# Optimization experiments

Hardware: AMD Instinct MI355X
Metric: run time of the kernel (lower is better)

Reference implementation:

```python
import jax, jax.numpy as jnp
import numpy as np

L1, L2 = 16, 16            # lattice shape -> translation group
N_SYMM = L1 * L2           # 256 group elements
IN_FEATURES = 32
FEATURES = 64
BATCH = 16


def translation_table(l1, l2):
    """Product table pt[g, h] = index of g^{-1} h for the 2D translation group."""
    n = l1 * l2
    g = np.arange(n)
    a, b = g // l2, g % l2          # coords of g
    c, d = a, b                     # coords of h (same enumeration)
    pt = ((c[None, :] - a[:, None]) % l1) * l2 + ((d[None, :] - b[:, None]) % l2)
    return jnp.asarray(pt, dtype=jnp.int32)  # (n_symm, n_symm)


def setup_inputs() -> dict:
    key = jax.random.key(0)
    kx, kk, kb = jax.random.split(key, 3)
    x = jax.random.normal(kx, (BATCH, IN_FEATURES, N_SYMM), dtype=jnp.float32)
    # default_equivariant_initializer ~ lecun normal, fan_in = in_features * kernel_size
    scale = 1.0 / np.sqrt(IN_FEATURES * N_SYMM)
    kernel = scale * jax.random.normal(kk, (FEATURES, IN_FEATURES, N_SYMM), dtype=jnp.float32)
    bias = jnp.zeros((FEATURES,), dtype=jnp.float32)
    product_table = translation_table(L1, L2)
    return {"x": x, "kernel": kernel, "bias": bias, "product_table": product_table}


def reference(x, kernel, bias, product_table):
    # Expand kernel via group product table: K[f, i, g, h] = kernel[f, i, pt[g, h]]
    # (feature_group_count = 1, mask = None so unmask is identity, kernel_size = n_symm)
    K = jnp.take(kernel, product_table, axis=2)          # (F, I, S, S) -- 536 MB fp32
    # dot_general contracts x dims (in_features, n_symm) with K dims (I, first S)
    out = jnp.einsum('big,figh->bfh', x, K)              # (B, F, S)
    out = out + bias[:, None]                            # bias broadcast over group dim
    return out
```

## Files before the change

### kernel.cpp

```cpp
#include <hip/hip_runtime.h>

typedef unsigned short u16;
typedef unsigned int u32;
typedef __attribute__((ext_vector_type(8))) short bfx8;
typedef __attribute__((ext_vector_type(4))) float fx4;
typedef __attribute__((ext_vector_type(4))) u32 ux4;
typedef __attribute__((ext_vector_type(2))) u32 ux2;

__device__ inline u32 f2bf(float v) {
  u32 u = __builtin_bit_cast(u32, v);
  u = (u + 0x7fffu + ((u >> 16) & 1u)) >> 16;
  return u;
}

__global__ __launch_bounds__(512, 4) void eq_main(const float* __restrict__ xin,
                                                  const float* __restrict__ kin,
                                                  float* __restrict__ part) {
  __shared__ __align__(16) char smem[74752];
  u16* As = (u16*)smem;
  u32* P4 = (u32*)(smem + 65536);
  u16* xraw = (u16*)(smem + 73728);
  float* red = (float*)smem;

  const int b = blockIdx.x & 15;
  const int hh = (blockIdx.x >> 4) & 1;
  const int ich = blockIdx.x >> 5;
  const int t = threadIdx.x;

  if (t < 128) {
    int iLoc = t >> 6, s4 = (t & 63) << 2;
    fx4 v = *(const fx4*)(xin + ((b << 5) + (ich << 1) + iLoc) * 256 + s4);
    ux2 p;
    p[0] = f2bf(v[0]) | (f2bf(v[1]) << 16);
    p[1] = f2bf(v[2]) | (f2bf(v[3]) << 16);
    *(ux2*)(xraw + iLoc * 256 + s4) = p;
  }

#pragma unroll
  for (int it = 0; it < 8; ++it) {
    int slot = it * 512 + t;
    int iLoc = slot >> 11;
    int f = (slot >> 5) & 63;
    int c = slot & 31;
    int cs = c ^ (f & 31);
    const float* src = kin + f * 8192 + ((ich << 1) + iLoc) * 256 + (cs << 3);
    fx4 v0 = *(const fx4*)src;
    fx4 v1 = *(const fx4*)(src + 4);
    ux4 p;
    p[0] = f2bf(v0[0]) | (f2bf(v0[1]) << 16);
    p[1] = f2bf(v0[2]) | (f2bf(v0[3]) << 16);
    p[2] = f2bf(v1[0]) | (f2bf(v1[1]) << 16);
    p[3] = f2bf(v1[2]) | (f2bf(v1[3]) << 16);
    *(ux4*)(As + slot * 8) = p;
  }
  __syncthreads();

  {
    int iLoc = t >> 8, e = t & 255;
    int r = e >> 4, par = (e >> 3) & 1, u0 = e & 7;
    const u16* xr = xraw + iLoc * 256 + (r << 4);
    ux4 q;
#pragma unroll
    for (int j = 0; j < 4; ++j) {
      int u = u0 + j;
      int c0 = (32 - 2 * u) & 15;
      u32 lo = xr[(c0 - par) & 15];
      u32 hi = xr[(c0 - par - 1) & 15];
      q[j] = lo | (hi << 16);
    }
    *(ux4*)(P4 + (t << 2)) = q;
  }
  __syncthreads();

  const int lane = t & 63;
  const int w = t >> 6;
  const int iLoc = w >> 2;
  const int wq = w & 3;
  const int n = lane & 15;
  const int quad = lane >> 4;
  const int s2_0 = (quad & 1) << 3;
  const int par = n & 1;
  const int u0 = ((s2_0 - n - par) & 15) >> 1;
  const int Pb4 = (iLoc << 10) + (par << 5) + (u0 << 2);
  const int s1q = quad >> 1;
  const u16* Aw = As + (iLoc << 14);
  const int Tbase = (hh << 3) + (wq << 1);

  fx4 acc[4][2];
#pragma unroll
  for (int a = 0; a < 4; ++a)
#pragma unroll
    for (int c = 0; c < 2; ++c) acc[a][c] = (fx4){0.f, 0.f, 0.f, 0.f};

#pragma unroll
  for (int kstep = 0; kstep < 8; ++kstep) {
    bfx8 af[4];
#pragma unroll
    for (int ft = 0; ft < 4; ++ft) {
      int f = (ft << 4) + n;
      int ch = ((kstep << 2) + quad) ^ (f & 31);
      af[ft] = *(const bfx8*)(Aw + f * 256 + ch * 8);
    }
    const int s1 = (kstep << 1) + s1q;
    bfx8 bfr[2];
#pragma unroll
    for (int ht = 0; ht < 2; ++ht) {
      int r = (Tbase + ht - s1) & 15;
      bfr[ht] = __builtin_bit_cast(bfx8, *(const ux4*)(P4 + (r << 6) + Pb4));
    }
#pragma unroll
    for (int ft = 0; ft < 4; ++ft)
#pragma unroll
      for (int ht = 0; ht < 2; ++ht)
        acc[ft][ht] =
            __builtin_amdgcn_mfma_f32_16x16x32_bf16(af[ft], bfr[ht], acc[ft][ht], 0, 0, 0);
  }

  __syncthreads();

  if (w >= 4) {
#pragma unroll
    for (int ft = 0; ft < 4; ++ft)
#pragma unroll
      for (int ht = 0; ht < 2; ++ht) {
        float* pr = &red[wq * 2176 + (ht * 16 + n) * 68 + (ft << 4) + (quad << 2)];
        *(fx4*)pr = acc[ft][ht];
      }
  }
  __syncthreads();
  if (w < 4) {
    float* pw = part + (((ich << 4) + b) << 14);
#pragma unroll
    for (int ft = 0; ft < 4; ++ft)
#pragma unroll
      for (int ht = 0; ht < 2; ++ht) {
        const float* pr = &red[wq * 2176 + (ht * 16 + n) * 68 + (ft << 4) + (quad << 2)];
        fx4 vv = *(const fx4*)pr;
        acc[ft][ht] = acc[ft][ht] + vv;
        int h = (hh << 7) + (wq << 5) + (ht << 4) + n;
#pragma unroll
        for (int reg = 0; reg < 4; ++reg) {
          int f = (ft << 4) + (quad << 2) + reg;
          pw[f * 256 + h] = acc[ft][ht][reg];
        }
      }
  }
}

__global__ __launch_bounds__(256) void eq_reduce(const float* __restrict__ part,
                                                 const float* __restrict__ bias,
                                                 float* __restrict__ out) {
  int o = (blockIdx.x * 256 + threadIdx.x) * 4;
  fx4 s = {0.f, 0.f, 0.f, 0.f};
#pragma unroll
  for (int i = 0; i < 16; ++i) s = s + *(const fx4*)(part + i * 262144 + o);
  float bv = bias[(o >> 8) & 63];
  s = s + (fx4){bv, bv, bv, bv};
  *(fx4*)(out + o) = s;
}

extern "C" void kernel_launch(void* const* d_in, const int* in_sizes, int n_in,
                              void* d_out, int out_size, void* d_ws, size_t ws_size,
                              hipStream_t stream) {
  (void)in_sizes; (void)n_in; (void)out_size; (void)ws_size;
  const float* x = (const float*)d_in[0];
  const float* k = (const float*)d_in[1];
  const float* bias = (const float*)d_in[2];
  float* part = (float*)d_ws;
  float* out = (float*)d_out;

  eq_main<<<512, 512, 0, stream>>>(x, k, part);
  eq_reduce<<<256, 256, 0, stream>>>(part, bias, out);
}
```

Baseline: 73.43 us.

## Fuse split-K reduction into main kernel via last-block atomic counter

```diff
diff --git a/kernel.cpp b/kernel.cpp
--- a/kernel.cpp
+++ b/kernel.cpp
@@ -13,14 +13,22 @@
   return u;
 }
 
+__global__ __launch_bounds__(64) void eq_init(u32* __restrict__ ctr) {
+  if (threadIdx.x < 32) ctr[threadIdx.x] = 0u;
+}
+
 __global__ __launch_bounds__(512, 4) void eq_main(const float* __restrict__ xin,
                                                   const float* __restrict__ kin,
-                                                  float* __restrict__ part) {
+                                                  const float* __restrict__ bias,
+                                                  float* __restrict__ part,
+                                                  u32* __restrict__ ctr,
+                                                  float* __restrict__ out) {
   __shared__ __align__(16) char smem[74752];
   u16* As = (u16*)smem;
   u32* P4 = (u32*)(smem + 65536);
   u16* xraw = (u16*)(smem + 73728);
   float* red = (float*)smem;
+  __shared__ int lastFlag;
 
   const int b = blockIdx.x & 15;
   const int hh = (blockIdx.x >> 4) & 1;
@@ -145,18 +153,31 @@
         }
       }
   }
-}
 
-__global__ __launch_bounds__(256) void eq_reduce(const float* __restrict__ part,
-                                                 const float* __restrict__ bias,
-                                                 float* __restrict__ out) {
-  int o = (blockIdx.x * 256 + threadIdx.x) * 4;
-  fx4 s = {0.f, 0.f, 0.f, 0.f};
+  __syncthreads();
+  if (t == 0) {
+    __threadfence();
+    u32 old = atomicAdd(&ctr[(b << 1) + hh], 1u);
+    lastFlag = (old == 15u);
+  }
+  __syncthreads();
+  if (lastFlag) {
+    __threadfence();
+    const int base = (hh << 7);
 #pragma unroll
-  for (int i = 0; i < 16; ++i) s = s + *(const fx4*)(part + i * 262144 + o);
-  float bv = bias[(o >> 8) & 63];
-  s = s + (fx4){bv, bv, bv, bv};
-  *(fx4*)(out + o) = s;
+    for (int j = 0; j < 4; ++j) {
+      int id = j * 512 + t;
+      int f = id >> 5;
+      int hl4 = (id & 31) << 2;
+      fx4 s = {0.f, 0.f, 0.f, 0.f};
+#pragma unroll
+      for (int c = 0; c < 16; ++c)
+        s = s + *(const fx4*)(part + (((c << 4) + b) << 14) + (f << 8) + base + hl4);
+      float bv = bias[f];
+      s = s + (fx4){bv, bv, bv, bv};
+      *(fx4*)(out + (b << 14) + (f << 8) + base + hl4) = s;
+    }
+  }
 }
 
 extern "C" void kernel_launch(void* const* d_in, const int* in_sizes, int n_in,
@@ -167,8 +188,9 @@
   const float* k = (const float*)d_in[1];
   const float* bias = (const float*)d_in[2];
   float* part = (float*)d_ws;
+  u32* ctr = (u32*)((char*)d_ws + 16u * 16u * 16384u * 4u);
   float* out = (float*)d_out;
 
-  eq_main<<<512, 512, 0, stream>>>(x, k, part);
-  eq_reduce<<<256, 256, 0, stream>>>(part, bias, out);
+  eq_init<<<1, 64, 0, stream>>>(ctr);
+  eq_main<<<512, 512, 0, stream>>>(x, k, bias, part, ctr, out);
 }
```

Result: slower. 100.9 us (+37.4%).

## Loop over more input channels per block to shrink partial-sum buffer

Applied to the files above, without the earlier changes.

```diff
diff --git a/kernel.cpp b/kernel.cpp
--- a/kernel.cpp
+++ b/kernel.cpp
@@ -16,59 +16,24 @@
 __global__ __launch_bounds__(512, 4) void eq_main(const float* __restrict__ xin,
                                                   const float* __restrict__ kin,
                                                   float* __restrict__ part) {
-  __shared__ __align__(16) char smem[74752];
+  __shared__ __align__(16) char smem[77824];
   u16* As = (u16*)smem;
   u32* P4 = (u32*)(smem + 65536);
   u16* xraw = (u16*)(smem + 73728);
   float* red = (float*)smem;
 
   const int b = blockIdx.x & 15;
-  const int hh = (blockIdx.x >> 4) & 1;
-  const int ich = blockIdx.x >> 5;
+  const int ichg = (blockIdx.x >> 4) & 3;
+  const int hq = blockIdx.x >> 6;
   const int t = threadIdx.x;
 
-  if (t < 128) {
+  {
     int iLoc = t >> 6, s4 = (t & 63) << 2;
-    fx4 v = *(const fx4*)(xin + ((b << 5) + (ich << 1) + iLoc) * 256 + s4);
+    fx4 v = *(const fx4*)(xin + ((b << 5) + (ichg << 3) + iLoc) * 256 + s4);
     ux2 p;
     p[0] = f2bf(v[0]) | (f2bf(v[1]) << 16);
     p[1] = f2bf(v[2]) | (f2bf(v[3]) << 16);
     *(ux2*)(xraw + iLoc * 256 + s4) = p;
-  }
-
-#pragma unroll
-  for (int it = 0; it < 8; ++it) {
-    int slot = it * 512 + t;
-    int iLoc = slot >> 11;
-    int f = (slot >> 5) & 63;
-    int c = slot & 31;
-    int cs = c ^ (f & 31);
-    const float* src = kin + f * 8192 + ((ich << 1) + iLoc) * 256 + (cs << 3);
-    fx4 v0 = *(const fx4*)src;
-    fx4 v1 = *(const fx4*)(src + 4);
-    ux4 p;
-    p[0] = f2bf(v0[0]) | (f2bf(v0[1]) << 16);
-    p[1] = f2bf(v0[2]) | (f2bf(v0[3]) << 16);
-    p[2] = f2bf(v1[0]) | (f2bf(v1[1]) << 16);
-    p[3] = f2bf(v1[2]) | (f2bf(v1[3]) << 16);
-    *(ux4*)(As + slot * 8) = p;
-  }
-  __syncthreads();
-
-  {
-    int iLoc = t >> 8, e = t & 255;
-    int r = e >> 4, par = (e >> 3) & 1, u0 = e & 7;
-    const u16* xr = xraw + iLoc * 256 + (r << 4);
-    ux4 q;
-#pragma unroll
-    for (int j = 0; j < 4; ++j) {
-      int u = u0 + j;
-      int c0 = (32 - 2 * u) & 15;
-      u32 lo = xr[(c0 - par) & 15];
-      u32 hi = xr[(c0 - par - 1) & 15];
-      q[j] = lo | (hi << 16);
-    }
-    *(ux4*)(P4 + (t << 2)) = q;
   }
   __syncthreads();
 
@@ -84,66 +49,88 @@
   const int Pb4 = (iLoc << 10) + (par << 5) + (u0 << 2);
   const int s1q = quad >> 1;
   const u16* Aw = As + (iLoc << 14);
-  const int Tbase = (hh << 3) + (wq << 1);
+  const int T = (hq << 2) + wq;
 
-  fx4 acc[4][2];
+  fx4 acc[4];
 #pragma unroll
-  for (int a = 0; a < 4; ++a)
+  for (int a = 0; a < 4; ++a) acc[a] = (fx4){0.f, 0.f, 0.f, 0.f};
+
+  for (int ic = 0; ic < 4; ++ic) {
 #pragma unroll
-    for (int c = 0; c < 2; ++c) acc[a][c] = (fx4){0.f, 0.f, 0.f, 0.f};
+    for (int it = 0; it < 8; ++it) {
+      int slot = it * 512 + t;
+      int iL = slot >> 11;
+      int f = (slot >> 5) & 63;
+      int c = slot & 31;
+      int cs = c ^ (f & 31);
+      const float* src = kin + f * 8192 + (((ichg << 2) + ic) * 2 + iL) * 256 + (cs << 3);
+      fx4 v0 = *(const fx4*)src;
+      fx4 v1 = *(const fx4*)(src + 4);
+      ux4 p;
+      p[0] = f2bf(v0[0]) | (f2bf(v0[1]) << 16);
+      p[1] = f2bf(v0[2]) | (f2bf(v0[3]) << 16);
+      p[2] = f2bf(v1[0]) | (f2bf(v1[1]) << 16);
+      p[3] = f2bf(v1[2]) | (f2bf(v1[3]) << 16);
+      *(ux4*)(As + slot * 8) = p;
+    }
+    {
+      int iL = t >> 8, e = t & 255;
+      int r = e >> 4, pr = (e >> 3) & 1, uu = e & 7;
+      const u16* xr = xraw + ((ic << 1) + iL) * 256 + (r << 4);
+      ux4 q;
+#pragma unroll
+      for (int j = 0; j < 4; ++j) {
+        int u = uu + j;
+        int c0 = (32 - 2 * u) & 15;
+        u32 lo = xr[(c0 - pr) & 15];
+        u32 hi = xr[(c0 - pr - 1) & 15];
+        q[j] = lo | (hi << 16);
+      }
+      *(ux4*)(P4 + (t << 2)) = q;
+    }
+    __syncthreads();
 
 #pragma unroll
-  for (int kstep = 0; kstep < 8; ++kstep) {
-    bfx8 af[4];
+    for (int kstep = 0; kstep < 8; ++kstep) {
+      bfx8 af[4];
 #pragma unroll
-    for (int ft = 0; ft < 4; ++ft) {
-      int f = (ft << 4) + n;
-      int ch = ((kstep << 2) + quad) ^ (f & 31);
-      af[ft] = *(const bfx8*)(Aw + f * 256 + ch * 8);
+      for (int ft = 0; ft < 4; ++ft) {
+        int f = (ft << 4) + n;
+        int ch = ((kstep << 2) + quad) ^ (f & 31);
+        af[ft] = *(const bfx8*)(Aw + f * 256 + ch * 8);
+      }
+      const int s1 = (kstep << 1) + s1q;
+      int r = (T - s1) & 15;
+      bfx8 bfr = __builtin_bit_cast(bfx8, *(const ux4*)(P4 + (r << 6) + Pb4));
+#pragma unroll
+      for (int ft = 0; ft < 4; ++ft)
+        acc[ft] = __builtin_amdgcn_mfma_f32_16x16x32_bf16(af[ft], bfr, acc[ft], 0, 0, 0);
     }
-    const int s1 = (kstep << 1) + s1q;
-    bfx8 bfr[2];
-#pragma unroll
-    for (int ht = 0; ht < 2; ++ht) {
-      int r = (Tbase + ht - s1) & 15;
-      bfr[ht] = __builtin_bit_cast(bfx8, *(const ux4*)(P4 + (r << 6) + Pb4));
-    }
-#pragma unroll
-    for (int ft = 0; ft < 4; ++ft)
-#pragma unroll
-      for (int ht = 0; ht < 2; ++ht)
-        acc[ft][ht] =
-            __builtin_amdgcn_mfma_f32_16x16x32_bf16(af[ft], bfr[ht], acc[ft][ht], 0, 0, 0);
+    __syncthreads();
   }
-
-  __syncthreads();
 
   if (w >= 4) {
 #pragma unroll
-    for (int ft = 0; ft < 4; ++ft)
-#pragma unroll
-      for (int ht = 0; ht < 2; ++ht) {
-        float* pr = &red[wq * 2176 + (ht * 16 + n) * 68 + (ft << 4) + (quad << 2)];
-        *(fx4*)pr = acc[ft][ht];
-      }
+    for (int ft = 0; ft < 4; ++ft) {
+      float* pr = &red[wq * 1088 + n * 68 + (ft << 4) + (quad << 2)];
+      *(fx4*)pr = acc[ft];
+    }
   }
   __syncthreads();
   if (w < 4) {
-    float* pw = part + (((ich << 4) + b) << 14);
+    float* pw = part + (((ichg << 4) + b) << 14);
 #pragma unroll
-    for (int ft = 0; ft < 4; ++ft)
+    for (int ft = 0; ft < 4; ++ft) {
+      const float* pr = &red[wq * 1088 + n * 68 + (ft << 4) + (quad << 2)];
+      fx4 vv = *(const fx4*)pr;
+      fx4 s = acc[ft] + vv;
+      int h = (hq << 6) + (wq << 4) + n;
 #pragma unroll
-      for (int ht = 0; ht < 2; ++ht) {
-        const float* pr = &red[wq * 2176 + (ht * 16 + n) * 68 + (ft << 4) + (quad << 2)];
-        fx4 vv = *(const fx4*)pr;
-        acc[ft][ht] = acc[ft][ht] + vv;
-        int h = (hh << 7) + (wq << 5) + (ht << 4) + n;
-#pragma unroll
-        for (int reg = 0; reg < 4; ++reg) {
-          int f = (ft << 4) + (quad << 2) + reg;
-          pw[f * 256 + h] = acc[ft][ht][reg];
-        }
+      for (int reg = 0; reg < 4; ++reg) {
+        int f = (ft << 4) + (quad << 2) + reg;
+        pw[f * 256 + h] = s[reg];
       }
+    }
   }
 }
 
@@ -153,7 +140,7 @@
   int o = (blockIdx.x * 256 + threadIdx.x) * 4;
   fx4 s = {0.f, 0.f, 0.f, 0.f};
 #pragma unroll
-  for (int i = 0; i < 16; ++i) s = s + *(const fx4*)(part + i * 262144 + o);
+  for (int i = 0; i < 4; ++i) s = s + *(const fx4*)(part + i * 262144 + o);
   float bv = bias[(o >> 8) & 63];
   s = s + (fx4){bv, bv, bv, bv};
   *(fx4*)(out + o) = s;
@@ -169,6 +156,6 @@
   float* part = (float*)d_ws;
   float* out = (float*)d_out;
 
-  eq_main<<<512, 512, 0, stream>>>(x, k, part);
+  eq_main<<<256, 512, 0, stream>>>(x, k, part);
   eq_reduce<<<256, 256, 0, stream>>>(part, bias, out);
 }
```

Result: slower. 80.67 us (+9.9%).
